# Kernel optimization log

Hardware: AMD Instinct MI355X
Metric: run time of the kernel (lower is better)

The kernel has to match this reference:

```python
import jax, jax.numpy as jnp
import numpy as np

VOCAB = 32000
EMB = 256
DEC = 1024
ENC = 1024  # 2 * encoder hidden (bi-directional)
B = 128
S = 512


def setup_inputs() -> dict:
    key = jax.random.key(0)
    ks = jax.random.split(key, 16)
    s = 0.02
    return {
        "inputs": jax.random.randint(ks[0], (B, 1), 0, VOCAB),
        "decoder_hidden": jax.random.normal(ks[1], (B, DEC), jnp.float32),
        "encoder_output": jax.random.normal(ks[2], (B, S, ENC), jnp.float32),
        "emb": jax.random.normal(ks[3], (VOCAB, EMB), jnp.float32) * s,
        "W1": jax.random.normal(ks[4], (ENC, DEC), jnp.float32) * s,
        "b1": jnp.zeros((DEC,), jnp.float32),
        "W2": jax.random.normal(ks[5], (DEC, DEC), jnp.float32) * s,
        "b2": jnp.zeros((DEC,), jnp.float32),
        "Wv": jax.random.normal(ks[6], (DEC, 1), jnp.float32) * s,
        "bv": jnp.zeros((1,), jnp.float32),
        "lstm_k": jax.random.normal(ks[7], (ENC + EMB, 4 * DEC), jnp.float32) * s,
        "lstm_rk": jax.random.normal(ks[8], (DEC, 4 * DEC), jnp.float32) * s,
        "lstm_b": jnp.zeros((4 * DEC,), jnp.float32),
        "fc_W": jax.random.normal(ks[9], (DEC, VOCAB), jnp.float32) * s,
        "fc_b": jnp.zeros((VOCAB,), jnp.float32),
    }


def reference(inputs, decoder_hidden, encoder_output, emb, W1, b1, W2, b2,
              Wv, bv, lstm_k, lstm_rk, lstm_b, fc_W, fc_b):
    # Bahdanau additive attention
    # score: (B, S, 1)
    hidden_proj = decoder_hidden @ W2 + b2                      # (B, DEC)
    score = jnp.tanh(encoder_output @ W1 + b1 + hidden_proj[:, None, :]) @ Wv + bv
    attention_weights = jax.nn.softmax(score, axis=1)           # (B, S, 1)
    context = jnp.sum(attention_weights * encoder_output, axis=1)  # (B, ENC)

    # embedding lookup of the single input token, concat [context, embed]
    x = jnp.concatenate([context, emb[inputs[:, 0]]], axis=-1)  # (B, ENC+EMB)

    # single-step LSTM. Original calls rnn(inputs) with NO initial_state,
    # so h0 = c0 = 0 and the recurrent kernel contributes nothing this step.
    z = x @ lstm_k + lstm_b + jnp.zeros((B, DEC), x.dtype) @ lstm_rk  # (B, 4*DEC)
    i, f, g, o = jnp.split(z, 4, axis=-1)  # keras gate order i,f,c,o
    c = jax.nn.sigmoid(f) * 0.0 + jax.nn.sigmoid(i) * jnp.tanh(g)
    h = jax.nn.sigmoid(o) * jnp.tanh(c)

    logits = h @ fc_W + fc_b                                    # (B, VOCAB)
    return logits, (h, c), attention_weights
```

## Files before the change

kernel.cpp:

```cpp
#include <hip/hip_runtime.h>
#include <hip/hip_bf16.h>
#include <stdint.h>

#define VOCAB 32000
#define EMB   256
#define DEC   1024
#define ENC   1024
#define BB    128
#define SS    512
#define MTOT  (BB * SS)
#define XCOLS (ENC + EMB)
#define NG    (4 * DEC)

typedef _Float16 half8  __attribute__((ext_vector_type(8)));
typedef _Float16 half4  __attribute__((ext_vector_type(4)));
typedef float    floatx4 __attribute__((ext_vector_type(4)));

__device__ __forceinline__ float fast_tanh(float x) {
    float e = __builtin_amdgcn_exp2f(x * 2.885390082f);
    return 1.0f - 2.0f * __builtin_amdgcn_rcpf(e + 1.0f);
}
__device__ __forceinline__ float fast_sigmoid(float x) {
    float e = __builtin_amdgcn_exp2f(-x * 1.442695041f);
    return __builtin_amdgcn_rcpf(1.0f + e);
}

__device__ __forceinline__ void gl_lds16(const void* g, void* l) {
    __builtin_amdgcn_global_load_lds(
        (const __attribute__((address_space(1))) uint32_t*)g,
        (__attribute__((address_space(3))) uint32_t*)l,
        16, 0, 0);
}

__global__ void k_transpose_w1(const float* __restrict__ W1, _Float16* __restrict__ w1t) {
    __shared__ float tile[32][33];
    const int k0 = blockIdx.y * 32, n0 = blockIdx.x * 32;
    const int tx = threadIdx.x, ty = threadIdx.y;
    #pragma unroll
    for (int j = 0; j < 4; ++j)
        tile[ty + j * 8][tx] = W1[(size_t)(k0 + ty + j * 8) * DEC + n0 + tx];
    __syncthreads();
    #pragma unroll
    for (int j = 0; j < 4; ++j)
        w1t[(size_t)(n0 + ty + j * 8) * ENC + k0 + tx] = (_Float16)tile[tx][ty + j * 8];
}

__global__ void k_convert(const float* __restrict__ src, _Float16* __restrict__ dst) {
    const int stride = gridDim.x * blockDim.x;
    const int n8 = (MTOT * ENC) / 8;
    for (int i = blockIdx.x * blockDim.x + threadIdx.x; i < n8; i += stride) {
        floatx4 a = ((const floatx4*)src)[2 * i];
        floatx4 b = ((const floatx4*)src)[2 * i + 1];
        half8 h;
        #pragma unroll
        for (int e = 0; e < 4; ++e) { h[e] = (_Float16)a[e]; h[e + 4] = (_Float16)b[e]; }
        ((half8*)dst)[i] = h;
    }
}

__global__ void k_hidden_proj(const float* __restrict__ dh, const float* __restrict__ W2,
                              const float* __restrict__ b1, const float* __restrict__ b2,
                              float* __restrict__ hp) {
    __shared__ float xs[8 * 1024];
    const int t = threadIdx.x;
    const int n = blockIdx.x * 128 + t;
    const int b0 = blockIdx.y * 8;
    for (int i = t; i < 2048; i += 128)
        ((floatx4*)xs)[i] = ((const floatx4*)(dh + (size_t)b0 * 1024))[i];
    __syncthreads();
    float acc[8] = {0, 0, 0, 0, 0, 0, 0, 0};
    for (int k = 0; k < 1024; ++k) {
        float wval = W2[(size_t)k * 1024 + n];
        #pragma unroll
        for (int j = 0; j < 8; ++j) acc[j] += xs[j * 1024 + k] * wval;
    }
    const float bias = b1[n] + b2[n];
    #pragma unroll
    for (int j = 0; j < 8; ++j) hp[(size_t)(b0 + j) * 1024 + n] = acc[j] + bias;
}

__global__ __launch_bounds__(256) void k_score_f16(
    const _Float16* __restrict__ ench, const _Float16* __restrict__ w1t,
    const float* __restrict__ hp, const float* __restrict__ wv,
    float* __restrict__ scores)
{
    __shared__ _Float16 As[128 * 32];
    __shared__ _Float16 Bs[128 * 32];
    const int g   = blockIdx.x;
    const int xcd = g & 7;
    const int n0  = ((g >> 3) & 7) * 128;
    const int m0  = ((xcd << 6) + (g >> 6)) << 7;
    const int b   = m0 >> 9;
    const int t = threadIdx.x;
    const int lane = t & 63, w = t >> 6;
    const int wm = (w >> 1) * 64, wn = (w & 1) * 64;
    const int col = lane & 15, q = lane >> 4;

    floatx4 acc[4][4];
    #pragma unroll
    for (int i = 0; i < 4; ++i)
        #pragma unroll
        for (int j = 0; j < 4; ++j) acc[i][j] = (floatx4){0.f, 0.f, 0.f, 0.f};

    const int srow = w * 32 + (lane >> 2);
    const int scol = (lane & 3) * 8;
    const _Float16* agp = ench + (size_t)(m0 + srow) * ENC + scol;
    const _Float16* bgp = w1t  + (size_t)(n0 + srow) * ENC + scol;
    _Float16* alp = &As[(w * 32) * 32];
    _Float16* blp = &Bs[(w * 32) * 32];

    for (int k0 = 0; k0 < ENC; k0 += 32) {
        __syncthreads();
        gl_lds16(agp + k0,                alp);
        gl_lds16(agp + k0 + (size_t)16 * ENC, alp + 16 * 32);
        gl_lds16(bgp + k0,                blp);
        gl_lds16(bgp + k0 + (size_t)16 * ENC, blp + 16 * 32);
        __syncthreads();
        half8 af[4], bf[4];
        #pragma unroll
        for (int i = 0; i < 4; ++i)
            af[i] = *(const half8*)(&As[(wm + i * 16 + col) * 32 + q * 8]);
        #pragma unroll
        for (int j = 0; j < 4; ++j)
            bf[j] = *(const half8*)(&Bs[(wn + j * 16 + col) * 32 + q * 8]);
        #pragma unroll
        for (int i = 0; i < 4; ++i)
            #pragma unroll
            for (int j = 0; j < 4; ++j)
                acc[i][j] = __builtin_amdgcn_mfma_f32_16x16x32_f16(af[i], bf[j], acc[i][j], 0, 0, 0);
    }

    float hpv[4], wvv[4];
    #pragma unroll
    for (int j = 0; j < 4; ++j) {
        int n = n0 + wn + j * 16 + col;
        hpv[j] = hp[b * 1024 + n];
        wvv[j] = wv[n];
    }
    #pragma unroll
    for (int i = 0; i < 4; ++i) {
        float rs0 = 0.f, rs1 = 0.f, rs2 = 0.f, rs3 = 0.f;
        #pragma unroll
        for (int j = 0; j < 4; ++j) {
            rs0 += fast_tanh(acc[i][j][0] + hpv[j]) * wvv[j];
            rs1 += fast_tanh(acc[i][j][1] + hpv[j]) * wvv[j];
            rs2 += fast_tanh(acc[i][j][2] + hpv[j]) * wvv[j];
            rs3 += fast_tanh(acc[i][j][3] + hpv[j]) * wvv[j];
        }
        #pragma unroll
        for (int off = 1; off < 16; off <<= 1) {
            rs0 += __shfl_xor(rs0, off);
            rs1 += __shfl_xor(rs1, off);
            rs2 += __shfl_xor(rs2, off);
            rs3 += __shfl_xor(rs3, off);
        }
        if (col == 0) {
            const int mrow = m0 + wm + i * 16 + q * 4;
            atomicAdd(&scores[mrow + 0], rs0);
            atomicAdd(&scores[mrow + 1], rs1);
            atomicAdd(&scores[mrow + 2], rs2);
            atomicAdd(&scores[mrow + 3], rs3);
        }
    }
}

__global__ __launch_bounds__(256) void k_score(
    const float* __restrict__ enc, const _Float16* __restrict__ w1t,
    const float* __restrict__ hp, const float* __restrict__ wv,
    float* __restrict__ scores)
{
    __shared__ _Float16 As[128 * 40];
    __shared__ _Float16 Bs[128 * 40];
    const int n0 = blockIdx.x * 128;
    const int m0 = blockIdx.y * 128;
    const int b  = m0 >> 9;
    const int t = threadIdx.x;
    const int lane = t & 63, w = t >> 6;
    const int wm = (w >> 1) * 64, wn = (w & 1) * 64;
    const int col = lane & 15, q = lane >> 4;

    floatx4 acc[4][4];
    #pragma unroll
    for (int i = 0; i < 4; ++i)
        #pragma unroll
        for (int j = 0; j < 4; ++j) acc[i][j] = (floatx4){0.f, 0.f, 0.f, 0.f};

    const int sr = t >> 1;
    const int sc = (t & 1) * 16;
    const float*    ag = enc + (size_t)(m0 + sr) * ENC + sc;
    const _Float16* bg = w1t + (size_t)(n0 + sr) * ENC + sc;
    _Float16* asw = &As[sr * 40 + sc];
    _Float16* bsw = &Bs[sr * 40 + sc];

    for (int k0 = 0; k0 < ENC; k0 += 32) {
        __syncthreads();
        floatx4 a0 = *(const floatx4*)(ag + k0);
        floatx4 a1 = *(const floatx4*)(ag + k0 + 4);
        floatx4 a2 = *(const floatx4*)(ag + k0 + 8);
        floatx4 a3 = *(const floatx4*)(ag + k0 + 12);
        half8 bv0 = *(const half8*)(bg + k0);
        half8 bv1 = *(const half8*)(bg + k0 + 8);
        half8 ha, hb;
        #pragma unroll
        for (int e = 0; e < 4; ++e) { ha[e] = (_Float16)a0[e]; ha[e + 4] = (_Float16)a1[e]; }
        #pragma unroll
        for (int e = 0; e < 4; ++e) { hb[e] = (_Float16)a2[e]; hb[e + 4] = (_Float16)a3[e]; }
        *(half8*)(asw)     = ha;
        *(half8*)(asw + 8) = hb;
        *(half8*)(bsw)     = bv0;
        *(half8*)(bsw + 8) = bv1;
        __syncthreads();
        half8 af[4], bf[4];
        #pragma unroll
        for (int i = 0; i < 4; ++i)
            af[i] = *(const half8*)(&As[(wm + i * 16 + col) * 40 + q * 8]);
        #pragma unroll
        for (int j = 0; j < 4; ++j)
            bf[j] = *(const half8*)(&Bs[(wn + j * 16 + col) * 40 + q * 8]);
        #pragma unroll
        for (int i = 0; i < 4; ++i)
            #pragma unroll
            for (int j = 0; j < 4; ++j)
                acc[i][j] = __builtin_amdgcn_mfma_f32_16x16x32_f16(af[i], bf[j], acc[i][j], 0, 0, 0);
    }

    float hpv[4], wvv[4];
    #pragma unroll
    for (int j = 0; j < 4; ++j) {
        int n = n0 + wn + j * 16 + col;
        hpv[j] = hp[b * 1024 + n];
        wvv[j] = wv[n];
    }
    #pragma unroll
    for (int i = 0; i < 4; ++i) {
        float rs0 = 0.f, rs1 = 0.f, rs2 = 0.f, rs3 = 0.f;
        #pragma unroll
        for (int j = 0; j < 4; ++j) {
            rs0 += fast_tanh(acc[i][j][0] + hpv[j]) * wvv[j];
            rs1 += fast_tanh(acc[i][j][1] + hpv[j]) * wvv[j];
            rs2 += fast_tanh(acc[i][j][2] + hpv[j]) * wvv[j];
            rs3 += fast_tanh(acc[i][j][3] + hpv[j]) * wvv[j];
        }
        #pragma unroll
        for (int off = 1; off < 16; off <<= 1) {
            rs0 += __shfl_xor(rs0, off);
            rs1 += __shfl_xor(rs1, off);
            rs2 += __shfl_xor(rs2, off);
            rs3 += __shfl_xor(rs3, off);
        }
        if (col == 0) {
            const int mrow = m0 + wm + i * 16 + q * 4;
            atomicAdd(&scores[mrow + 0], rs0);
            atomicAdd(&scores[mrow + 1], rs1);
            atomicAdd(&scores[mrow + 2], rs2);
            atomicAdd(&scores[mrow + 3], rs3);
        }
    }
}

__global__ void k_softmax_emb(const float* __restrict__ scores, const int* __restrict__ tok,
                              const float* __restrict__ emb, float* __restrict__ aw,
                              float* __restrict__ x) {
    const int b = blockIdx.x, t = threadIdx.x;
    float s0 = scores[b * SS + t];
    float s1 = scores[b * SS + 256 + t];
    float mx = fmaxf(s0, s1);
    for (int off = 32; off; off >>= 1) mx = fmaxf(mx, __shfl_xor(mx, off));
    __shared__ float redm[4], reds[4];
    const int w = t >> 6, lane = t & 63;
    if (lane == 0) redm[w] = mx;
    __syncthreads();
    mx = fmaxf(fmaxf(redm[0], redm[1]), fmaxf(redm[2], redm[3]));
    float e0 = exp2f((s0 - mx) * 1.44269504f);
    float e1 = exp2f((s1 - mx) * 1.44269504f);
    float sm = e0 + e1;
    for (int off = 32; off; off >>= 1) sm += __shfl_xor(sm, off);
    if (lane == 0) reds[w] = sm;
    __syncthreads();
    sm = reds[0] + reds[1] + reds[2] + reds[3];
    const float inv = 1.0f / sm;
    aw[b * SS + t]       = e0 * inv;
    aw[b * SS + 256 + t] = e1 * inv;
    x[(size_t)b * XCOLS + ENC + t] = emb[(size_t)tok[b] * EMB + t];
}

__global__ void k_context(const float* __restrict__ enc, const float* __restrict__ aw,
                          float* __restrict__ x) {
    const int b = blockIdx.x >> 2;
    const int e = (blockIdx.x & 3) * 256 + threadIdx.x;
    const float* ep = enc + (size_t)b * SS * ENC + e;
    const float* ap = aw + b * SS;
    float acc = 0.f;
    #pragma unroll 8
    for (int s = 0; s < SS; ++s) acc += ap[s] * ep[(size_t)s * ENC];
    x[(size_t)b * XCOLS + e] = acc;
}

__global__ void k_lstm(const float* __restrict__ x, const float* __restrict__ lk,
                       float* __restrict__ z) {
    __shared__ float xs[8 * XCOLS];
    const int t = threadIdx.x;
    const int n = blockIdx.x * 128 + t;
    const int b0 = blockIdx.y * 8;
    for (int i = t; i < 2560; i += 128)
        ((floatx4*)xs)[i] = ((const floatx4*)(x + (size_t)b0 * XCOLS))[i];
    __syncthreads();
    float acc[8] = {0, 0, 0, 0, 0, 0, 0, 0};
    for (int k = 0; k < XCOLS; ++k) {
        float wval = lk[(size_t)k * NG + n];
        #pragma unroll
        for (int j = 0; j < 8; ++j) acc[j] += xs[j * XCOLS + k] * wval;
    }
    #pragma unroll
    for (int j = 0; j < 8; ++j) z[(size_t)(b0 + j) * NG + n] = acc[j];
}

__global__ void k_gates(const float* __restrict__ z, const float* __restrict__ lb,
                        float* __restrict__ h_out, float* __restrict__ c_out) {
    const int idx = blockIdx.x * 256 + threadIdx.x;
    const int b = idx >> 10, d = idx & 1023;
    const float* zb = z + (size_t)b * NG;
    float iv = zb[d]        + lb[d];
    float gv = zb[d + 2048] + lb[d + 2048];
    float ov = zb[d + 3072] + lb[d + 3072];
    float c = fast_sigmoid(iv) * fast_tanh(gv);
    float h = fast_sigmoid(ov) * fast_tanh(c);
    h_out[idx] = h;
    c_out[idx] = c;
}

__global__ __launch_bounds__(256) void k_fc(
    const float* __restrict__ hsrc, const float* __restrict__ fcW,
    const float* __restrict__ fcb, float* __restrict__ logits)
{
    __shared__ _Float16 As[128 * 40];
    __shared__ _Float16 Bs[128 * 40];
    const int n0 = blockIdx.x * 128;
    const int t = threadIdx.x;
    const int lane = t & 63, w = t >> 6;
    const int wm = (w >> 1) * 64, wn = (w & 1) * 64;
    const int col = lane & 15, q = lane >> 4;

    floatx4 acc[4][4];
    #pragma unroll
    for (int i = 0; i < 4; ++i)
        #pragma unroll
        for (int j = 0; j < 4; ++j) acc[i][j] = (floatx4){0.f, 0.f, 0.f, 0.f};

    const int sr = t >> 1, sc = (t & 1) * 16;
    const float* ag = hsrc + (size_t)sr * 1024 + sc;
    _Float16* asw = &As[sr * 40 + sc];
    const int bn = (t & 31) * 4;
    const int bk = (t >> 5) * 4;

    for (int k0 = 0; k0 < 1024; k0 += 32) {
        __syncthreads();
        floatx4 a0 = *(const floatx4*)(ag + k0);
        floatx4 a1 = *(const floatx4*)(ag + k0 + 4);
        floatx4 a2 = *(const floatx4*)(ag + k0 + 8);
        floatx4 a3 = *(const floatx4*)(ag + k0 + 12);
        half8 ha, hb;
        #pragma unroll
        for (int e = 0; e < 4; ++e) { ha[e] = (_Float16)a0[e]; ha[e + 4] = (_Float16)a1[e]; }
        #pragma unroll
        for (int e = 0; e < 4; ++e) { hb[e] = (_Float16)a2[e]; hb[e + 4] = (_Float16)a3[e]; }
        *(half8*)(asw)     = ha;
        *(half8*)(asw + 8) = hb;
        floatx4 w0 = *(const floatx4*)(fcW + (size_t)(k0 + bk + 0) * VOCAB + n0 + bn);
        floatx4 w1 = *(const floatx4*)(fcW + (size_t)(k0 + bk + 1) * VOCAB + n0 + bn);
        floatx4 w2 = *(const floatx4*)(fcW + (size_t)(k0 + bk + 2) * VOCAB + n0 + bn);
        floatx4 w3 = *(const floatx4*)(fcW + (size_t)(k0 + bk + 3) * VOCAB + n0 + bn);
        #pragma unroll
        for (int c = 0; c < 4; ++c) {
            half4 p = { (_Float16)w0[c], (_Float16)w1[c], (_Float16)w2[c], (_Float16)w3[c] };
            *(half4*)(&Bs[(bn + c) * 40 + bk]) = p;
        }
        __syncthreads();
        half8 af[4], bf[4];
        #pragma unroll
        for (int i = 0; i < 4; ++i)
            af[i] = *(const half8*)(&As[(wm + i * 16 + col) * 40 + q * 8]);
        #pragma unroll
        for (int j = 0; j < 4; ++j)
            bf[j] = *(const half8*)(&Bs[(wn + j * 16 + col) * 40 + q * 8]);
        #pragma unroll
        for (int i = 0; i < 4; ++i)
            #pragma unroll
            for (int j = 0; j < 4; ++j)
                acc[i][j] = __builtin_amdgcn_mfma_f32_16x16x32_f16(af[i], bf[j], acc[i][j], 0, 0, 0);
    }

    float fcbv[4];
    #pragma unroll
    for (int j = 0; j < 4; ++j) fcbv[j] = fcb[n0 + wn + j * 16 + col];
    #pragma unroll
    for (int i = 0; i < 4; ++i)
        #pragma unroll
        for (int j = 0; j < 4; ++j)
            #pragma unroll
            for (int r = 0; r < 4; ++r) {
                const int row = wm + i * 16 + q * 4 + r;
                logits[(size_t)row * VOCAB + n0 + wn + j * 16 + col] = acc[i][j][r] + fcbv[j];
            }
}

extern "C" void kernel_launch(void* const* d_in, const int* in_sizes, int n_in,
                              void* d_out, int out_size, void* d_ws, size_t ws_size,
                              hipStream_t stream) {
    const int*   tok    = (const int*)d_in[0];
    const float* dh     = (const float*)d_in[1];
    const float* enc    = (const float*)d_in[2];
    const float* emb    = (const float*)d_in[3];
    const float* W1     = (const float*)d_in[4];
    const float* b1     = (const float*)d_in[5];
    const float* W2     = (const float*)d_in[6];
    const float* b2     = (const float*)d_in[7];
    const float* Wv     = (const float*)d_in[8];
    const float* lstm_k = (const float*)d_in[10];
    const float* lstm_b = (const float*)d_in[12];
    const float* fc_W   = (const float*)d_in[13];
    const float* fc_b   = (const float*)d_in[14];

    float* out    = (float*)d_out;
    float* logits = out;
    float* h_out  = out + 4096000;
    float* c_out  = out + 4096000 + 131072;
    float* aw     = out + 4096000 + 262144;

    char* ws = (char*)d_ws;
    _Float16* w1t    = (_Float16*)ws;
    float*    hp     = (float*)(ws + 2097152);
    float*    scores = (float*)(ws + 2621440);
    float*    x      = (float*)(ws + 2883584);
    float*    z      = (float*)(ws + 3538944);
    _Float16* ench   = (_Float16*)(ws + 6291456);

    const size_t need_fast = 6291456 + (size_t)MTOT * ENC * sizeof(_Float16);
    const bool fast = ws_size >= need_fast;

    hipMemsetAsync(scores, 0, MTOT * sizeof(float), stream);
    k_transpose_w1<<<dim3(32, 32), dim3(32, 8), 0, stream>>>(W1, w1t);
    k_hidden_proj<<<dim3(8, 16), 128, 0, stream>>>(dh, W2, b1, b2, hp);
    if (fast) {
        k_convert<<<2048, 256, 0, stream>>>(enc, ench);
        k_score_f16<<<4096, 256, 0, stream>>>(ench, w1t, hp, Wv, scores);
    } else {
        k_score<<<dim3(8, 512), 256, 0, stream>>>(enc, w1t, hp, Wv, scores);
    }
    k_softmax_emb<<<128, 256, 0, stream>>>(scores, tok, emb, aw, x);
    k_context<<<512, 256, 0, stream>>>(enc, aw, x);
    k_lstm<<<dim3(32, 16), 128, 0, stream>>>(x, lstm_k, z);
    k_gates<<<512, 256, 0, stream>>>(z, lstm_b, h_out, c_out);
    k_fc<<<250, 256, 0, stream>>>(h_out, fc_W, fc_b, logits);
}
```

Before: 975.5 us.

## Split-K small GEMMs with atomics, double-buffer score GEMM, vectorize context reduction

The hidden projection and LSTM GEMMs now split the K dimension across a third grid axis and accumulate with atomicAdd into zeroed buffers, which raises block count for these low-occupancy kernels. The score MFMA kernel gains double-buffered LDS staging so the next tile loads while the current one computes, with one barrier per iteration. The context reduction now splits the sequence across blocks and uses float4 loads, also accumulating via atomics. In exchange it adds memsets and atomic traffic, and makes the summation order nondeterministic.

```diff
diff --git a/kernel.cpp b/kernel.cpp
--- a/kernel.cpp
+++ b/kernel.cpp
@@ -61,22 +61,26 @@
 __global__ void k_hidden_proj(const float* __restrict__ dh, const float* __restrict__ W2,
                               const float* __restrict__ b1, const float* __restrict__ b2,
                               float* __restrict__ hp) {
-    __shared__ float xs[8 * 1024];
+    __shared__ float xs[8 * 128];
     const int t = threadIdx.x;
     const int n = blockIdx.x * 128 + t;
     const int b0 = blockIdx.y * 8;
-    for (int i = t; i < 2048; i += 128)
-        ((floatx4*)xs)[i] = ((const floatx4*)(dh + (size_t)b0 * 1024))[i];
+    const int k0 = blockIdx.z * 128;
+    for (int i = t; i < 1024; i += 128) {
+        const int j = i >> 7, kk = i & 127;
+        xs[i] = dh[(size_t)(b0 + j) * 1024 + k0 + kk];
+    }
     __syncthreads();
     float acc[8] = {0, 0, 0, 0, 0, 0, 0, 0};
-    for (int k = 0; k < 1024; ++k) {
-        float wval = W2[(size_t)k * 1024 + n];
-        #pragma unroll
-        for (int j = 0; j < 8; ++j) acc[j] += xs[j * 1024 + k] * wval;
-    }
-    const float bias = b1[n] + b2[n];
-    #pragma unroll
-    for (int j = 0; j < 8; ++j) hp[(size_t)(b0 + j) * 1024 + n] = acc[j] + bias;
+    for (int k = 0; k < 128; ++k) {
+        float wval = W2[(size_t)(k0 + k) * 1024 + n];
+        #pragma unroll
+        for (int j = 0; j < 8; ++j) acc[j] += xs[j * 128 + k] * wval;
+    }
+    const float bias = (blockIdx.z == 0) ? (b1[n] + b2[n]) : 0.0f;
+    #pragma unroll
+    for (int j = 0; j < 8; ++j)
+        atomicAdd(&hp[(size_t)(b0 + j) * 1024 + n], acc[j] + bias);
 }
 
 __global__ __launch_bounds__(256) void k_score_f16(
@@ -84,8 +88,8 @@
     const float* __restrict__ hp, const float* __restrict__ wv,
     float* __restrict__ scores)
 {
-    __shared__ _Float16 As[128 * 32];
-    __shared__ _Float16 Bs[128 * 32];
+    __shared__ _Float16 As[2][128 * 32];
+    __shared__ _Float16 Bs[2][128 * 32];
     const int g   = blockIdx.x;
     const int xcd = g & 7;
     const int n0  = ((g >> 3) & 7) * 128;
@@ -106,29 +110,40 @@
     const int scol = (lane & 3) * 8;
     const _Float16* agp = ench + (size_t)(m0 + srow) * ENC + scol;
     const _Float16* bgp = w1t  + (size_t)(n0 + srow) * ENC + scol;
-    _Float16* alp = &As[(w * 32) * 32];
-    _Float16* blp = &Bs[(w * 32) * 32];
-
-    for (int k0 = 0; k0 < ENC; k0 += 32) {
-        __syncthreads();
-        gl_lds16(agp + k0,                alp);
-        gl_lds16(agp + k0 + (size_t)16 * ENC, alp + 16 * 32);
-        gl_lds16(bgp + k0,                blp);
-        gl_lds16(bgp + k0 + (size_t)16 * ENC, blp + 16 * 32);
-        __syncthreads();
+    const int lofs = (w * 32) * 32;
+
+    #define STAGE(buf, kk) do {                         \
+        gl_lds16(agp + (kk),              &As[buf][lofs]);           \
+        gl_lds16(agp + (kk) + 16 * ENC,   &As[buf][lofs + 16 * 32]); \
+        gl_lds16(bgp + (kk),              &Bs[buf][lofs]);           \
+        gl_lds16(bgp + (kk) + 16 * ENC,   &Bs[buf][lofs + 16 * 32]); \
+    } while (0)
+
+    STAGE(0, 0);
+    asm volatile("s_waitcnt vmcnt(0)" ::: "memory");
+    __builtin_amdgcn_s_barrier();
+
+    for (int it = 0; it < 32; ++it) {
+        const int cur = it & 1;
+        if (it < 31) STAGE(cur ^ 1, (it + 1) * 32);
         half8 af[4], bf[4];
         #pragma unroll
         for (int i = 0; i < 4; ++i)
-            af[i] = *(const half8*)(&As[(wm + i * 16 + col) * 32 + q * 8]);
+            af[i] = *(const half8*)(&As[cur][(wm + i * 16 + col) * 32 + q * 8]);
         #pragma unroll
         for (int j = 0; j < 4; ++j)
-            bf[j] = *(const half8*)(&Bs[(wn + j * 16 + col) * 32 + q * 8]);
+            bf[j] = *(const half8*)(&Bs[cur][(wn + j * 16 + col) * 32 + q * 8]);
         #pragma unroll
         for (int i = 0; i < 4; ++i)
             #pragma unroll
             for (int j = 0; j < 4; ++j)
                 acc[i][j] = __builtin_amdgcn_mfma_f32_16x16x32_f16(af[i], bf[j], acc[i][j], 0, 0, 0);
-    }
+        if (it < 31) {
+            asm volatile("s_waitcnt vmcnt(0)" ::: "memory");
+            __builtin_amdgcn_s_barrier();
+        }
+    }
+    #undef STAGE
 
     float hpv[4], wvv[4];
     #pragma unroll
@@ -286,33 +301,46 @@
 
 __global__ void k_context(const float* __restrict__ enc, const float* __restrict__ aw,
                           float* __restrict__ x) {
-    const int b = blockIdx.x >> 2;
-    const int e = (blockIdx.x & 3) * 256 + threadIdx.x;
-    const float* ep = enc + (size_t)b * SS * ENC + e;
-    const float* ap = aw + b * SS;
-    float acc = 0.f;
-    #pragma unroll 8
-    for (int s = 0; s < SS; ++s) acc += ap[s] * ep[(size_t)s * ENC];
-    x[(size_t)b * XCOLS + e] = acc;
+    const int b  = blockIdx.x >> 2;
+    const int s0 = (blockIdx.x & 3) * 128;
+    const int e4 = threadIdx.x;
+    const float* ep = enc + ((size_t)b * SS + s0) * ENC;
+    const float* ap = aw + b * SS + s0;
+    float a0 = 0.f, a1 = 0.f, a2 = 0.f, a3 = 0.f;
+    #pragma unroll 4
+    for (int s = 0; s < 128; ++s) {
+        const float a = ap[s];
+        floatx4 v = ((const floatx4*)(ep + (size_t)s * ENC))[e4];
+        a0 += a * v[0]; a1 += a * v[1]; a2 += a * v[2]; a3 += a * v[3];
+    }
+    float* xp = x + (size_t)b * XCOLS + e4 * 4;
+    atomicAdd(xp + 0, a0);
+    atomicAdd(xp + 1, a1);
+    atomicAdd(xp + 2, a2);
+    atomicAdd(xp + 3, a3);
 }
 
 __global__ void k_lstm(const float* __restrict__ x, const float* __restrict__ lk,
                        float* __restrict__ z) {
-    __shared__ float xs[8 * XCOLS];
+    __shared__ float xs[8 * 320];
     const int t = threadIdx.x;
     const int n = blockIdx.x * 128 + t;
     const int b0 = blockIdx.y * 8;
-    for (int i = t; i < 2560; i += 128)
-        ((floatx4*)xs)[i] = ((const floatx4*)(x + (size_t)b0 * XCOLS))[i];
+    const int k0 = blockIdx.z * 320;
+    #pragma unroll
+    for (int j = 0; j < 8; ++j)
+        for (int kk = t; kk < 320; kk += 128)
+            xs[j * 320 + kk] = x[(size_t)(b0 + j) * XCOLS + k0 + kk];
     __syncthreads();
     float acc[8] = {0, 0, 0, 0, 0, 0, 0, 0};
-    for (int k = 0; k < XCOLS; ++k) {
-        float wval = lk[(size_t)k * NG + n];
-        #pragma unroll
-        for (int j = 0; j < 8; ++j) acc[j] += xs[j * XCOLS + k] * wval;
-    }
-    #pragma unroll
-    for (int j = 0; j < 8; ++j) z[(size_t)(b0 + j) * NG + n] = acc[j];
+    for (int k = 0; k < 320; ++k) {
+        float wval = lk[(size_t)(k0 + k) * NG + n];
+        #pragma unroll
+        for (int j = 0; j < 8; ++j) acc[j] += xs[j * 320 + k] * wval;
+    }
+    #pragma unroll
+    for (int j = 0; j < 8; ++j)
+        atomicAdd(&z[(size_t)(b0 + j) * NG + n], acc[j]);
 }
 
 __global__ void k_gates(const float* __restrict__ z, const float* __restrict__ lb,
@@ -439,8 +467,12 @@
     const bool fast = ws_size >= need_fast;
 
     hipMemsetAsync(scores, 0, MTOT * sizeof(float), stream);
+    hipMemsetAsync(hp, 0, BB * DEC * sizeof(float), stream);
+    hipMemsetAsync(x, 0, (size_t)BB * XCOLS * sizeof(float), stream);
+    hipMemsetAsync(z, 0, (size_t)BB * NG * sizeof(float), stream);
+
     k_transpose_w1<<<dim3(32, 32), dim3(32, 8), 0, stream>>>(W1, w1t);
-    k_hidden_proj<<<dim3(8, 16), 128, 0, stream>>>(dh, W2, b1, b2, hp);
+    k_hidden_proj<<<dim3(8, 16, 8), 128, 0, stream>>>(dh, W2, b1, b2, hp);
     if (fast) {
         k_convert<<<2048, 256, 0, stream>>>(enc, ench);
         k_score_f16<<<4096, 256, 0, stream>>>(ench, w1t, hp, Wv, scores);
@@ -449,7 +481,7 @@
     }
     k_softmax_emb<<<128, 256, 0, stream>>>(scores, tok, emb, aw, x);
     k_context<<<512, 256, 0, stream>>>(enc, aw, x);
-    k_lstm<<<dim3(32, 16), 128, 0, stream>>>(x, lstm_k, z);
+    k_lstm<<<dim3(32, 16, 4), 128, 0, stream>>>(x, lstm_k, z);
     k_gates<<<512, 256, 0, stream>>>(z, lstm_b, h_out, c_out);
     k_fc<<<250, 256, 0, stream>>>(h_out, fc_W, fc_b, logits);
 }
```

After: 888.8 us. -8.9%, faster.
